# Optimization experiments

Measured on AMD Instinct MI355X. Metric: run time of the kernel, lower is better.

Reference implementation:

```python
import jax, jax.numpy as jnp
import numpy as np
from jax import lax

DIM = 256
HEADS = 8
HIDDEN = int(DIM * 2.66)  # 680
KS = 3


def conv1x1(x, w, b):
    # x: (B,C,H,W), w: (O,C), b: (O,)
    return jnp.einsum('oc,bchw->bohw', w, x) + b[None, :, None, None]


def dwconv(x, w, b):
    # depthwise 3x3, SAME padding; w: (C,1,3,3)
    y = lax.conv_general_dilated(
        x, w, window_strides=(1, 1), padding='SAME',
        feature_group_count=x.shape[1],
        dimension_numbers=('NCHW', 'OIHW', 'NCHW'))
    return y + b[None, :, None, None]


def layernorm_c(x, w, b, eps=1e-5):
    # torch nn.LayerNorm(dim) applied on NHWC -> normalize over channel dim
    mu = jnp.mean(x, axis=1, keepdims=True)
    var = jnp.mean(jnp.square(x - mu), axis=1, keepdims=True)
    xn = (x - mu) * lax.rsqrt(var + eps)
    return xn * w[None, :, None, None] + b[None, :, None, None]


def l2norm(x, eps=1e-12):
    # F.normalize(dim=-1)
    n = jnp.sqrt(jnp.sum(jnp.square(x), axis=-1, keepdims=True))
    return x / jnp.maximum(n, eps)


def setup_inputs() -> dict:
    key = jax.random.key(0)
    ks = jax.random.split(key, 20)
    s = 0.02
    d = {
        'x': jax.random.normal(ks[0], (4, DIM, 128, 128), jnp.float32),
        'n1_w': jnp.ones((DIM,), jnp.float32),
        'n1_b': jnp.zeros((DIM,), jnp.float32),
        'temp': jnp.ones((HEADS, 1, 1), jnp.float32),
        'qkv_w': jax.random.normal(ks[1], (3 * DIM, DIM), jnp.float32) * s,
        'qkv_b': jnp.zeros((3 * DIM,), jnp.float32),
        'qkv_dw_w': jax.random.normal(ks[2], (3 * DIM, 1, KS, KS), jnp.float32) * s,
        'qkv_dw_b': jnp.zeros((3 * DIM,), jnp.float32),
        'attn_po_w': jax.random.normal(ks[3], (DIM, DIM), jnp.float32) * s,
        'attn_po_b': jnp.zeros((DIM,), jnp.float32),
        'n2_w': jnp.ones((DIM,), jnp.float32),
        'n2_b': jnp.zeros((DIM,), jnp.float32),
        'pin_w': jax.random.normal(ks[4], (2 * HIDDEN, DIM), jnp.float32) * s,
        'pin_b': jnp.zeros((2 * HIDDEN,), jnp.float32),
        'dw_w': jax.random.normal(ks[5], (2 * HIDDEN, 1, KS, KS), jnp.float32) * s,
        'dw_b': jnp.zeros((2 * HIDDEN,), jnp.float32),
        'pout_w': jax.random.normal(ks[6], (DIM, HIDDEN), jnp.float32) * s,
        'pout_b': jnp.zeros((DIM,), jnp.float32),
    }
    return d


def attention(x, temp, qkv_w, qkv_b, qkv_dw_w, qkv_dw_b, po_w, po_b):
    B, C, H, W = x.shape
    qkv = dwconv(conv1x1(x, qkv_w, qkv_b), qkv_dw_w, qkv_dw_b)  # (B,3C,H,W)
    q, k, v = jnp.split(qkv, 3, axis=1)
    hd = C // HEADS
    q = l2norm(q.reshape(B, HEADS, hd, H * W))
    k = l2norm(k.reshape(B, HEADS, hd, H * W))
    v = v.reshape(B, HEADS, hd, H * W)
    attn = jnp.einsum('bhcn,bhdn->bhcd', q, k) * temp  # (B,h,hd,hd) channel attn
    attn = jax.nn.softmax(attn, axis=-1)
    out = jnp.einsum('bhcd,bhdn->bhcn', attn, v).reshape(B, C, H, W)
    return conv1x1(out, po_w, po_b)


def ffn(x, pin_w, pin_b, dw_w, dw_b, pout_w, pout_b):
    y = dwconv(conv1x1(x, pin_w, pin_b), dw_w, dw_b)
    y1, y2 = jnp.split(y, 2, axis=1)
    y = y1 * jax.nn.gelu(y2, approximate=False)
    return conv1x1(y, pout_w, pout_b)


def reference(x, n1_w, n1_b, temp, qkv_w, qkv_b, qkv_dw_w, qkv_dw_b,
              attn_po_w, attn_po_b, n2_w, n2_b, pin_w, pin_b, dw_w, dw_b,
              pout_w, pout_b):
    x = x + attention(layernorm_c(x, n1_w, n1_b), temp, qkv_w, qkv_b,
                      qkv_dw_w, qkv_dw_b, attn_po_w, attn_po_b)
    x = x + ffn(layernorm_c(x, n2_w, n2_b), pin_w, pin_b, dw_w, dw_b,
                pout_w, pout_b)
    return x
```

## Files before the change

kernel.cpp:

```cpp
#include <hip/hip_runtime.h>
#include <hip/hip_bf16.h>

#define NPIX 16384
#define BATCH 4
#define DIM 256
#define HEADS 8
#define HD 32
#define CHQKV 768
#define HID 680
#define HID2 1360

typedef __attribute__((ext_vector_type(8))) short short8v;
typedef __attribute__((ext_vector_type(4))) float float4v;

__device__ __forceinline__ ushort bf_hi(float v) {
    unsigned u = __float_as_uint(v);
    u += 0x7fffu + ((u >> 16) & 1u);
    return (ushort)(u >> 16);
}
__device__ __forceinline__ float bf_tof(ushort h) {
    return __uint_as_float(((unsigned)h) << 16);
}
__device__ __forceinline__ void bf_split(float v, ushort &h, ushort &l) {
    h = bf_hi(v);
    l = bf_hi(v - bf_tof(h));
}

__global__ void zero_kernel(float* __restrict__ p, int n) {
    int i = blockIdx.x * blockDim.x + threadIdx.x;
    if (i < n) p[i] = 0.f;
}

__global__ void convert_weights(const float* __restrict__ qkv_w, const float* __restrict__ po_w,
                                const float* __restrict__ pin_w, const float* __restrict__ pout_w,
                                ushort* __restrict__ qH, ushort* __restrict__ qL,
                                ushort* __restrict__ oH, ushort* __restrict__ oL,
                                ushort* __restrict__ iH, ushort* __restrict__ iL,
                                ushort* __restrict__ uH, ushort* __restrict__ uL) {
    int i = blockIdx.x * 256 + threadIdx.x;
    const float* s; ushort *dh, *dl; int off;
    if (i < 196608)      { s = qkv_w;  dh = qH; dl = qL; off = i; }
    else if (i < 262144) { s = po_w;   dh = oH; dl = oL; off = i - 196608; }
    else if (i < 610304) { s = pin_w;  dh = iH; dl = iL; off = i - 262144; }
    else if (i < 784384) { s = pout_w; dh = uH; dl = uL; off = i - 610304; }
    else return;
    ushort h, l; bf_split(s[off], h, l);
    dh[off] = h; dl[off] = l;
}

__global__ void ln_fused(const float* __restrict__ x, const float* __restrict__ lw,
                         const float* __restrict__ lb, uint* __restrict__ XH,
                         uint* __restrict__ XL) {
    __shared__ float Ss[256], Ss2[256], muS[64], rsS[64], wS[256], bS[256];
    int t = threadIdx.x, px = t & 63, cg = t >> 6, c0 = cg * 64;
    int p = blockIdx.x * 64 + px;
    wS[t] = lw[t]; bS[t] = lb[t];
    float v[64]; float s = 0.f, s2 = 0.f;
    #pragma unroll
    for (int j = 0; j < 64; ++j) {
        v[j] = x[(size_t)(c0 + j) * NPIX + p];
        s += v[j]; s2 += v[j] * v[j];
    }
    Ss[t] = s; Ss2[t] = s2;
    __syncthreads();
    if (t < 64) {
        float ts = Ss[t] + Ss[t + 64] + Ss[t + 128] + Ss[t + 192];
        float t2 = Ss2[t] + Ss2[t + 64] + Ss2[t + 128] + Ss2[t + 192];
        float m = ts * (1.0f / DIM);
        float var = t2 * (1.0f / DIM) - m * m;
        muS[t] = m; rsS[t] = rsqrtf(var + 1e-5f);
    }
    __syncthreads();
    float m = muS[px], r = rsS[px];
    #pragma unroll
    for (int j = 0; j < 64; j += 2) {
        float a = (v[j] - m) * r * wS[c0 + j] + bS[c0 + j];
        float b2 = (v[j + 1] - m) * r * wS[c0 + j + 1] + bS[c0 + j + 1];
        ushort h0, l0, h1, l1; bf_split(a, h0, l0); bf_split(b2, h1, l1);
        size_t w = (size_t)((c0 + j) >> 1) * NPIX + p;
        XH[w] = (uint)h0 | ((uint)h1 << 16);
        XL[w] = (uint)l0 | ((uint)l1 << 16);
    }
}

template <int NT, bool RES>
__global__ void gemm_mfma(const ushort* __restrict__ WH, const ushort* __restrict__ WL,
                          const uint* __restrict__ BpH, const uint* __restrict__ BpL,
                          const float* __restrict__ bias, const float* __restrict__ res,
                          float* __restrict__ Out, int M, int K, int ksteps) {
    constexpr int NI = NT / 32;
    constexpr int CPT = NT / 16;
    constexpr int NU = CPT / 4;
    constexpr int LDSW = NT * 20;
    __shared__ uint BhL[2][LDSW];
    __shared__ uint BlL[2][LDSW];
    __shared__ float biasS[128];
    const int N = NPIX;
    int tid = threadIdx.x;
    int m0 = blockIdx.y * 128;
    int n0 = blockIdx.x * NT;
    int l = tid & 63;
    int wid = tid >> 6;
    int wr = wid >> 1, wc = wid & 1;
    int lr = l & 15, lk = l >> 4;
    int kp = tid & 15;
    int cb = (tid >> 4) * CPT;

    if (tid < 128) biasS[tid] = (m0 + tid < M) ? bias[m0 + tid] : 0.f;

    float4v acc[4][NI];
    #pragma unroll
    for (int i = 0; i < 4; ++i)
        #pragma unroll
        for (int j = 0; j < NI; ++j) acc[i][j] = (float4v)0.f;

    const int Kh = K >> 1;
    uint4 sh[NU], sl[NU];

    auto LOADB = [&](int ks) {
        int kpg = ks * 16 + kp;
        bool kin = kpg < Kh;
        int kpc = kin ? kpg : (Kh - 1);
        const uint* ph = &BpH[(size_t)kpc * N + n0 + cb];
        const uint* pl = &BpL[(size_t)kpc * N + n0 + cb];
        #pragma unroll
        for (int u = 0; u < NU; ++u) {
            sh[u] = *(const uint4*)(ph + 4 * u);
            sl[u] = *(const uint4*)(pl + 4 * u);
        }
        if (!kin) {
            #pragma unroll
            for (int u = 0; u < NU; ++u) {
                sh[u] = make_uint4(0, 0, 0, 0);
                sl[u] = make_uint4(0, 0, 0, 0);
            }
        }
    };
    auto STOREB = [&](int buf) {
        #pragma unroll
        for (int u = 0; u < NU; ++u) {
            int base = (cb + 4 * u) * 20 + kp;
            BhL[buf][base     ] = sh[u].x;
            BhL[buf][base + 20] = sh[u].y;
            BhL[buf][base + 40] = sh[u].z;
            BhL[buf][base + 60] = sh[u].w;
            BlL[buf][base     ] = sl[u].x;
            BlL[buf][base + 20] = sl[u].y;
            BlL[buf][base + 40] = sl[u].z;
            BlL[buf][base + 60] = sl[u].w;
        }
    };

    LOADB(0);
    STOREB(0);
    __syncthreads();
    int cur = 0;

    for (int ks = 0; ks < ksteps; ++ks) {
        bool more = (ks + 1) < ksteps;
        if (more) LOADB(ks + 1);

        short8v ah[4], al[4];
        int kk = ks * 32 + lk * 8;
        bool kok = (kk + 7) < K;
        int kc = kok ? kk : 0;
        #pragma unroll
        for (int mi = 0; mi < 4; ++mi) {
            int arow = m0 + wr * 64 + mi * 16 + lr;
            bool ok = (arow < M) && kok;
            int arc = arow < M ? arow : (M - 1);
            short8v th = *(const short8v*)&WH[(size_t)arc * K + kc];
            short8v tl = *(const short8v*)&WL[(size_t)arc * K + kc];
            short8v z = (short8v)0;
            ah[mi] = ok ? th : z;
            al[mi] = ok ? tl : z;
        }
        short8v bh[NI], bl[NI];
        #pragma unroll
        for (int ni = 0; ni < NI; ++ni) {
            int brow = wc * (NI * 16) + ni * 16 + lr;
            bh[ni] = *(const short8v*)&BhL[cur][brow * 20 + lk * 4];
            bl[ni] = *(const short8v*)&BlL[cur][brow * 20 + lk * 4];
        }
        #pragma unroll
        for (int mi = 0; mi < 4; ++mi)
            #pragma unroll
            for (int ni = 0; ni < NI; ++ni) {
                acc[mi][ni] = __builtin_amdgcn_mfma_f32_16x16x32_bf16(ah[mi], bh[ni], acc[mi][ni], 0, 0, 0);
                acc[mi][ni] = __builtin_amdgcn_mfma_f32_16x16x32_bf16(ah[mi], bl[ni], acc[mi][ni], 0, 0, 0);
                acc[mi][ni] = __builtin_amdgcn_mfma_f32_16x16x32_bf16(al[mi], bh[ni], acc[mi][ni], 0, 0, 0);
            }
        if (more) {
            STOREB(cur ^ 1);
            __syncthreads();
            cur ^= 1;
        }
    }

    int lr4 = lk * 4;
    #pragma unroll
    for (int mi = 0; mi < 4; ++mi) {
        #pragma unroll
        for (int ni = 0; ni < NI; ++ni) {
            int rloc = wr * 64 + mi * 16 + lr4;
            int col = n0 + wc * (NI * 16) + ni * 16 + lr;
            #pragma unroll
            for (int r = 0; r < 4; ++r) {
                int row = m0 + rloc + r;
                if (row < M) {
                    float v = acc[mi][ni][r] + biasS[rloc + r];
                    size_t o = (size_t)row * N + col;
                    if (RES) v += res[o];
                    Out[o] = v;
                }
            }
        }
    }
}

__global__ void dwconv_sumsq(const float* __restrict__ in, const float* __restrict__ w9,
                             const float* __restrict__ bias, float* __restrict__ out,
                             float* __restrict__ ssq, float* __restrict__ ssk) {
    __shared__ float T[34][132];
    __shared__ float red[256];
    int bid = blockIdx.x;
    int ch = bid >> 2, rt = bid & 3;
    int g0 = rt * 32;
    int t = threadIdx.x;
    const float* src = in + (size_t)ch * NPIX;
    int c4 = (t & 31) * 4;
    for (int rr = t >> 5; rr < 34; rr += 8) {
        int grow = g0 - 1 + rr;
        float4 v = make_float4(0.f, 0.f, 0.f, 0.f);
        if (grow >= 0 && grow < 128) v = *(const float4*)&src[grow * 128 + c4];
        *(float4*)&T[rr][c4 + 1] = v;
    }
    if (t < 34) { T[t][0] = 0.f; T[t][129] = 0.f; }
    float wgt[9];
    #pragma unroll
    for (int i = 0; i < 9; ++i) wgt[i] = w9[ch * 9 + i];
    float bi = bias[ch];
    __syncthreads();
    int w = t & 127;
    int jb = (t >> 7) * 16;
    float a0 = T[jb][w], a1 = T[jb][w + 1], a2 = T[jb][w + 2];
    float b0 = T[jb + 1][w], b1 = T[jb + 1][w + 1], b2 = T[jb + 1][w + 2];
    float sq = 0.f;
    float* dst = out + (size_t)ch * NPIX + (g0 + jb) * 128 + w;
    #pragma unroll
    for (int i = 0; i < 16; ++i) {
        float c0 = T[jb + i + 2][w], c1 = T[jb + i + 2][w + 1], c2 = T[jb + i + 2][w + 2];
        float acc = bi + wgt[0] * a0 + wgt[1] * a1 + wgt[2] * a2
                       + wgt[3] * b0 + wgt[4] * b1 + wgt[5] * b2
                       + wgt[6] * c0 + wgt[7] * c1 + wgt[8] * c2;
        dst[i * 128] = acc;
        sq += acc * acc;
        a0 = b0; a1 = b1; a2 = b2; b0 = c0; b1 = c1; b2 = c2;
    }
    if (ch < 512) {
        red[t] = sq;
        __syncthreads();
        for (int st = 128; st > 0; st >>= 1) {
            if (t < st) red[t] += red[t + st];
            __syncthreads();
        }
        if (t == 0) {
            float* d2 = (ch < DIM) ? &ssq[ch] : &ssk[ch - DIM];
            atomicAdd(d2, red[0]);
        }
    }
}

__global__ void gram_kernel(const float* __restrict__ qkv, float* __restrict__ G) {
    int hH = blockIdx.x;
    int n0 = blockIdx.y * 512;
    __shared__ float qs[32][68];
    __shared__ float ks[32][68];
    int tid = threadIdx.x;
    int c = tid >> 3;
    int lo = (tid & 7) * 8;
    int dbase = tid & 7;
    const float* qbase = qkv + ((size_t)hH * HD + c) * NPIX;
    const float* kbase = qbase + (size_t)DIM * NPIX;
    float acc[4] = {0.f, 0.f, 0.f, 0.f};
    for (int t0 = 0; t0 < 512; t0 += 64) {
        __syncthreads();
        *(float4*)&qs[c][lo]     = *(const float4*)&qbase[n0 + t0 + lo];
        *(float4*)&qs[c][lo + 4] = *(const float4*)&qbase[n0 + t0 + lo + 4];
        *(float4*)&ks[c][lo]     = *(const float4*)&kbase[n0 + t0 + lo];
        *(float4*)&ks[c][lo + 4] = *(const float4*)&kbase[n0 + t0 + lo + 4];
        __syncthreads();
        for (int t = 0; t < 64; ++t) {
            float qv = qs[c][t];
            #pragma unroll
            for (int j = 0; j < 4; ++j) acc[j] += qv * ks[dbase + 8 * j][t];
        }
    }
    float* Gb = G + hH * 1024 + c * 32;
    #pragma unroll
    for (int j = 0; j < 4; ++j) atomicAdd(&Gb[dbase + 8 * j], acc[j]);
}

__global__ void attn_softmax(const float* __restrict__ G, const float* __restrict__ ssq,
                             const float* __restrict__ ssk, const float* __restrict__ temp,
                             float* __restrict__ A) {
    int hH = blockIdx.x;
    int tid = threadIdx.x;
    int c = tid >> 5, d = tid & 31;
    float nq = fmaxf(sqrtf(ssq[hH * HD + c]), 1e-12f);
    float nk = fmaxf(sqrtf(ssk[hH * HD + d]), 1e-12f);
    float v = G[hH * 1024 + c * 32 + d] / (nq * nk) * temp[hH];
    float m = v;
    #pragma unroll
    for (int s = 1; s < 32; s <<= 1) m = fmaxf(m, __shfl_xor(m, s, 32));
    float e = expf(v - m);
    float ssum = e;
    #pragma unroll
    for (int s = 1; s < 32; s <<= 1) ssum += __shfl_xor(ssum, s, 32);
    A[hH * 1024 + c * 32 + d] = e / ssum;
}

__global__ void pv_kernel(const float* __restrict__ A, const float* __restrict__ qkv,
                          uint* __restrict__ VH, uint* __restrict__ VL) {
    int hH = blockIdx.x;
    int n = blockIdx.y * 256 + threadIdx.x;
    __shared__ float As[1024];
    for (int i = threadIdx.x; i < 1024; i += 256) As[i] = A[hH * 1024 + i];
    __syncthreads();
    const float* vbase = qkv + ((size_t)(512 + hH * HD)) * NPIX + n;
    float vv[32];
    #pragma unroll
    for (int d = 0; d < 32; ++d) vv[d] = vbase[(size_t)d * NPIX];
    #pragma unroll
    for (int cc = 0; cc < 32; cc += 2) {
        float a0 = 0.f, a1 = 0.f;
        #pragma unroll
        for (int d = 0; d < 32; ++d) {
            a0 += As[cc * 32 + d] * vv[d];
            a1 += As[cc * 32 + 32 + d] * vv[d];
        }
        ushort h0, l0, h1, l1; bf_split(a0, h0, l0); bf_split(a1, h1, l1);
        size_t w = (size_t)((hH * HD + cc) >> 1) * NPIX + n;
        VH[w] = (uint)h0 | ((uint)h1 << 16);
        VL[w] = (uint)l0 | ((uint)l1 << 16);
    }
}

__global__ void dwgate(const float* __restrict__ in, const float* __restrict__ w9,
                       const float* __restrict__ bias, uint* __restrict__ GH,
                       uint* __restrict__ GL) {
    __shared__ float T[4][18][132];
    int bid = blockIdx.x;
    int cp = bid >> 3, rt = bid & 7;
    int c0 = cp * 2;
    int g0 = rt * 16;
    int t = threadIdx.x;
    for (int idx = t; idx < 4 * 18 * 32; idx += 256) {
        int pl = idx / 576;
        int rem = idx - pl * 576;
        int rr = rem >> 5;
        int cc4 = (rem & 31) * 4;
        int ch = c0 + (pl & 1) + (pl >> 1) * HID;
        int grow = g0 - 1 + rr;
        float4 v = make_float4(0.f, 0.f, 0.f, 0.f);
        if (grow >= 0 && grow < 128)
            v = *(const float4*)&in[(size_t)ch * NPIX + grow * 128 + cc4];
        *(float4*)&T[pl][rr][cc4 + 1] = v;
    }
    if (t < 72) {
        int pl = t / 18, rr = t % 18;
        T[pl][rr][0] = 0.f; T[pl][rr][129] = 0.f;
    }
    float wg[4][9]; float bs[4];
    #pragma unroll
    for (int p = 0; p < 4; ++p) {
        int ch = c0 + (p & 1) + (p >> 1) * HID;
        bs[p] = bias[ch];
        #pragma unroll
        for (int i = 0; i < 9; ++i) wg[p][i] = w9[ch * 9 + i];
    }
    __syncthreads();
    int w = t & 127;
    int jb = (t >> 7) * 8;
    float A[4][3], B[4][3];
    #pragma unroll
    for (int p = 0; p < 4; ++p) {
        A[p][0] = T[p][jb][w];     A[p][1] = T[p][jb][w + 1];     A[p][2] = T[p][jb][w + 2];
        B[p][0] = T[p][jb + 1][w]; B[p][1] = T[p][jb + 1][w + 1]; B[p][2] = T[p][jb + 1][w + 2];
    }
    size_t wbase = (size_t)cp * NPIX + (g0 + jb) * 128 + w;
    #pragma unroll
    for (int i = 0; i < 8; ++i) {
        float o[4];
        #pragma unroll
        for (int p = 0; p < 4; ++p) {
            float cA = T[p][jb + i + 2][w], cB = T[p][jb + i + 2][w + 1], cC = T[p][jb + i + 2][w + 2];
            o[p] = bs[p] + wg[p][0] * A[p][0] + wg[p][1] * A[p][1] + wg[p][2] * A[p][2]
                         + wg[p][3] * B[p][0] + wg[p][4] * B[p][1] + wg[p][5] * B[p][2]
                         + wg[p][6] * cA + wg[p][7] * cB + wg[p][8] * cC;
            A[p][0] = B[p][0]; A[p][1] = B[p][1]; A[p][2] = B[p][2];
            B[p][0] = cA; B[p][1] = cB; B[p][2] = cC;
        }
        float g0f = 0.5f * o[2] * (1.0f + erff(o[2] * 0.70710678118654752f));
        float g1f = 0.5f * o[3] * (1.0f + erff(o[3] * 0.70710678118654752f));
        float r0 = o[0] * g0f, r1 = o[1] * g1f;
        ushort h0, l0, h1, l1; bf_split(r0, h0, l0); bf_split(r1, h1, l1);
        GH[wbase + i * 128] = (uint)h0 | ((uint)h1 << 16);
        GL[wbase + i * 128] = (uint)l0 | ((uint)l1 << 16);
    }
}

extern "C" void kernel_launch(void* const* d_in, const int* in_sizes, int n_in,
                              void* d_out, int out_size, void* d_ws, size_t ws_size,
                              hipStream_t stream) {
    const float* x        = (const float*)d_in[0];
    const float* n1w      = (const float*)d_in[1];
    const float* n1b      = (const float*)d_in[2];
    const float* temp     = (const float*)d_in[3];
    const float* qkv_w    = (const float*)d_in[4];
    const float* qkv_b    = (const float*)d_in[5];
    const float* qkv_dw_w = (const float*)d_in[6];
    const float* qkv_dw_b = (const float*)d_in[7];
    const float* po_w     = (const float*)d_in[8];
    const float* po_b     = (const float*)d_in[9];
    const float* n2w      = (const float*)d_in[10];
    const float* n2b      = (const float*)d_in[11];
    const float* pin_w    = (const float*)d_in[12];
    const float* pin_b    = (const float*)d_in[13];
    const float* dw_w     = (const float*)d_in[14];
    const float* dw_b     = (const float*)d_in[15];
    const float* pout_w   = (const float*)d_in[16];
    const float* pout_b   = (const float*)d_in[17];
    float* out = (float*)d_out;

    char* ws = (char*)d_ws;
    float* R0 = (float*)ws;
    char*  R1c = ws + 50331648;
    float* R1 = (float*)R1c;
    float* R2 = (float*)(ws + 100663296);
    char*  wb = ws + 189792256;
    ushort* WqkvH = (ushort*)wb;
    ushort* WqkvL = WqkvH + 196608;
    ushort* WpoH  = WqkvL + 196608;
    ushort* WpoL  = WpoH + 65536;
    ushort* WpinH = WpoL + 65536;
    ushort* WpinL = WpinH + 348160;
    ushort* WpoutH = WpinL + 348160;
    ushort* WpoutL = WpoutH + 174080;
    float* G     = (float*)(wb + 3137536);
    float* ssq   = G + 8192;
    float* ssk   = ssq + 256;
    float* attnA = ssk + 256;
    uint* XHp = (uint*)R1c;
    uint* XLp = XHp + 2097152;
    uint* VHp = (uint*)R1c;
    uint* VLp = XLp;
    uint* GHp = (uint*)R1c;
    uint* GLp = GHp + 5570560;

    convert_weights<<<3064, 256, 0, stream>>>(qkv_w, po_w, pin_w, pout_w,
                                              WqkvH, WqkvL, WpoH, WpoL,
                                              WpinH, WpinL, WpoutH, WpoutL);

    for (int b = 0; b < BATCH; ++b) {
        const float* xb = x + (size_t)b * DIM * NPIX;
        float* outb = out + (size_t)b * DIM * NPIX;

        ln_fused<<<256, 256, 0, stream>>>(xb, n1w, n1b, XHp, XLp);
        gemm_mfma<128, false><<<dim3(128, 6), 256, 0, stream>>>(
            WqkvH, WqkvL, XHp, XLp, qkv_b, nullptr, R0, CHQKV, DIM, 8);
        zero_kernel<<<34, 256, 0, stream>>>(G, 8704);
        dwconv_sumsq<<<CHQKV * 4, 256, 0, stream>>>(R0, qkv_dw_w, qkv_dw_b, R1, ssq, ssk);
        gram_kernel<<<dim3(8, 32), 256, 0, stream>>>(R1, G);
        attn_softmax<<<8, 1024, 0, stream>>>(G, ssq, ssk, temp, attnA);
        pv_kernel<<<dim3(8, 64), 256, 0, stream>>>(attnA, R1, VHp, VLp);
        gemm_mfma<64, true><<<dim3(256, 2), 256, 0, stream>>>(
            WpoH, WpoL, VHp, VLp, po_b, xb, outb, DIM, DIM, 8);

        ln_fused<<<256, 256, 0, stream>>>(outb, n2w, n2b, XHp, XLp);
        gemm_mfma<128, false><<<dim3(128, 11), 256, 0, stream>>>(
            WpinH, WpinL, XHp, XLp, pin_b, nullptr, R2, HID2, DIM, 8);
        dwgate<<<340 * 8, 256, 0, stream>>>(R2, dw_w, dw_b, GHp, GLp);
        gemm_mfma<64, true><<<dim3(256, 2), 256, 0, stream>>>(
            WpoutH, WpoutL, GHp, GLp, pout_b, outb, outb, DIM, HID, 22);
    }
}
```

Before: 1.569 ms.

## Coalesce B-tile global loads and prefetch A fragments one k-step ahead

The B-tile load mapping changes so that threads in a row read contiguous columns: each thread loads uint4 chunks across several k-pair rows instead of several column chunks for a single k-pair. The LDS row stride goes from 20 to 21 words to match the new store pattern and avoid bank conflicts. The A-operand (weight) fragments are now double-buffered in registers, loaded one k-step ahead alongside B, to hide global latency behind the MFMAs. This raises register pressure and could reduce occupancy.

Measured after the change: 2.561 ms. 1.63x slower.

```diff
diff --git a/kernel.cpp b/kernel.cpp
--- a/kernel.cpp
+++ b/kernel.cpp
@@ -89,9 +89,10 @@
                           const float* __restrict__ bias, const float* __restrict__ res,
                           float* __restrict__ Out, int M, int K, int ksteps) {
     constexpr int NI = NT / 32;
-    constexpr int CPT = NT / 16;
-    constexpr int NU = CPT / 4;
-    constexpr int LDSW = NT * 20;
+    constexpr int TPR = NT / 4;
+    constexpr int RPP = 1024 / NT;
+    constexpr int NU = 16 / RPP;
+    constexpr int LDSW = NT * 21;
     __shared__ uint BhL[2][LDSW];
     __shared__ uint BlL[2][LDSW];
     __shared__ float biasS[128];
@@ -103,8 +104,8 @@
     int wid = tid >> 6;
     int wr = wid >> 1, wc = wid & 1;
     int lr = l & 15, lk = l >> 4;
-    int kp = tid & 15;
-    int cb = (tid >> 4) * CPT;
+    int rw = tid / TPR;
+    int c4 = (tid % TPR) * 4;
 
     if (tid < 128) biasS[tid] = (m0 + tid < M) ? bias[m0 + tid] : 0.f;
 
@@ -116,21 +117,18 @@
 
     const int Kh = K >> 1;
     uint4 sh[NU], sl[NU];
+    short8v ahC[4], alC[4], ahN[4], alN[4];
 
     auto LOADB = [&](int ks) {
-        int kpg = ks * 16 + kp;
-        bool kin = kpg < Kh;
-        int kpc = kin ? kpg : (Kh - 1);
-        const uint* ph = &BpH[(size_t)kpc * N + n0 + cb];
-        const uint* pl = &BpL[(size_t)kpc * N + n0 + cb];
         #pragma unroll
         for (int u = 0; u < NU; ++u) {
-            sh[u] = *(const uint4*)(ph + 4 * u);
-            sl[u] = *(const uint4*)(pl + 4 * u);
-        }
-        if (!kin) {
-            #pragma unroll
-            for (int u = 0; u < NU; ++u) {
+            int r = rw + u * RPP;
+            int kpg = ks * 16 + r;
+            bool kin = kpg < Kh;
+            int kpc = kin ? kpg : (Kh - 1);
+            sh[u] = *(const uint4*)&BpH[(size_t)kpc * N + n0 + c4];
+            sl[u] = *(const uint4*)&BpL[(size_t)kpc * N + n0 + c4];
+            if (!kin) {
                 sh[u] = make_uint4(0, 0, 0, 0);
                 sl[u] = make_uint4(0, 0, 0, 0);
             }
@@ -139,28 +137,18 @@
     auto STOREB = [&](int buf) {
         #pragma unroll
         for (int u = 0; u < NU; ++u) {
-            int base = (cb + 4 * u) * 20 + kp;
-            BhL[buf][base     ] = sh[u].x;
-            BhL[buf][base + 20] = sh[u].y;
-            BhL[buf][base + 40] = sh[u].z;
-            BhL[buf][base + 60] = sh[u].w;
-            BlL[buf][base     ] = sl[u].x;
-            BlL[buf][base + 20] = sl[u].y;
-            BlL[buf][base + 40] = sl[u].z;
-            BlL[buf][base + 60] = sl[u].w;
+            int r = rw + u * RPP;
+            BhL[buf][(c4 + 0) * 21 + r] = sh[u].x;
+            BhL[buf][(c4 + 1) * 21 + r] = sh[u].y;
+            BhL[buf][(c4 + 2) * 21 + r] = sh[u].z;
+            BhL[buf][(c4 + 3) * 21 + r] = sh[u].w;
+            BlL[buf][(c4 + 0) * 21 + r] = sl[u].x;
+            BlL[buf][(c4 + 1) * 21 + r] = sl[u].y;
+            BlL[buf][(c4 + 2) * 21 + r] = sl[u].z;
+            BlL[buf][(c4 + 3) * 21 + r] = sl[u].w;
         }
     };
-
-    LOADB(0);
-    STOREB(0);
-    __syncthreads();
-    int cur = 0;
-
-    for (int ks = 0; ks < ksteps; ++ks) {
-        bool more = (ks + 1) < ksteps;
-        if (more) LOADB(ks + 1);
-
-        short8v ah[4], al[4];
+    auto LOADA = [&](int ks, short8v (&ah)[4], short8v (&al)[4]) {
         int kk = ks * 32 + lk * 8;
         bool kok = (kk + 7) < K;
         int kc = kok ? kk : 0;
@@ -175,25 +163,41 @@
             ah[mi] = ok ? th : z;
             al[mi] = ok ? tl : z;
         }
+    };
+
+    LOADB(0);
+    LOADA(0, ahC, alC);
+    STOREB(0);
+    __syncthreads();
+    int cur = 0;
+
+    for (int ks = 0; ks < ksteps; ++ks) {
+        bool more = (ks + 1) < ksteps;
+        if (more) {
+            LOADB(ks + 1);
+            LOADA(ks + 1, ahN, alN);
+        }
         short8v bh[NI], bl[NI];
         #pragma unroll
         for (int ni = 0; ni < NI; ++ni) {
             int brow = wc * (NI * 16) + ni * 16 + lr;
-            bh[ni] = *(const short8v*)&BhL[cur][brow * 20 + lk * 4];
-            bl[ni] = *(const short8v*)&BlL[cur][brow * 20 + lk * 4];
+            bh[ni] = *(const short8v*)&BhL[cur][brow * 21 + lk * 4];
+            bl[ni] = *(const short8v*)&BlL[cur][brow * 21 + lk * 4];
         }
         #pragma unroll
         for (int mi = 0; mi < 4; ++mi)
             #pragma unroll
             for (int ni = 0; ni < NI; ++ni) {
-                acc[mi][ni] = __builtin_amdgcn_mfma_f32_16x16x32_bf16(ah[mi], bh[ni], acc[mi][ni], 0, 0, 0);
-                acc[mi][ni] = __builtin_amdgcn_mfma_f32_16x16x32_bf16(ah[mi], bl[ni], acc[mi][ni], 0, 0, 0);
-                acc[mi][ni] = __builtin_amdgcn_mfma_f32_16x16x32_bf16(al[mi], bh[ni], acc[mi][ni], 0, 0, 0);
+                acc[mi][ni] = __builtin_amdgcn_mfma_f32_16x16x32_bf16(ahC[mi], bh[ni], acc[mi][ni], 0, 0, 0);
+                acc[mi][ni] = __builtin_amdgcn_mfma_f32_16x16x32_bf16(ahC[mi], bl[ni], acc[mi][ni], 0, 0, 0);
+                acc[mi][ni] = __builtin_amdgcn_mfma_f32_16x16x32_bf16(alC[mi], bh[ni], acc[mi][ni], 0, 0, 0);
             }
         if (more) {
             STOREB(cur ^ 1);
             __syncthreads();
             cur ^= 1;
+            #pragma unroll
+            for (int mi = 0; mi < 4; ++mi) { ahC[mi] = ahN[mi]; alC[mi] = alN[mi]; }
         }
     }
 
```
